# Kernel tuning notes

Hardware: AMD Instinct MI355X
Metric: run time of the kernel (lower is better)

## Reference

```python
import jax, jax.numpy as jnp
import numpy as np

B, L, D, H = 64, 256, 512, 512


def setup_inputs() -> dict:
    key = jax.random.key(0)
    ks = jax.random.split(key, 17)
    s = 1.0 / np.sqrt(D + H)  # torch nn.Linear default init bound

    def w(k):
        return jax.random.uniform(k, (H, D + H), minval=-s, maxval=s, dtype=jnp.float32)

    def b(k):
        return jax.random.uniform(k, (H,), minval=-s, maxval=s, dtype=jnp.float32)

    inp = {"x": jax.random.normal(ks[0], (B, L, D), dtype=jnp.float32)}
    names = ["f", "i", "o", "g"]
    idx = 1
    for d in ("fw", "bw"):
        for n in names:
            kw, kb = jax.random.split(ks[idx])
            inp[f"W_{d}_{n}"] = w(kw)
            inp[f"b_{d}_{n}"] = b(kb)
            idx += 1
    return inp


def _make_cell(Wf, bf, Wi, bi, Wo, bo, Wg, bg):
    def cell(carry, xt):
        h, c = carry
        comb = jnp.concatenate([xt, h], axis=1)  # (B, D+H)
        ft = jax.nn.sigmoid(comb @ Wf.T + bf)
        it = jax.nn.sigmoid(comb @ Wi.T + bi)
        ot = jax.nn.sigmoid(comb @ Wo.T + bo)
        gt = jnp.tanh(comb @ Wg.T + bg)
        c = ft * c + it * gt
        h = ot * jnp.tanh(c)
        return (h, c), h
    return cell


def reference(x, W_fw_f, b_fw_f, W_fw_i, b_fw_i, W_fw_o, b_fw_o, W_fw_g, b_fw_g,
              W_bw_f, b_bw_f, W_bw_i, b_bw_i, W_bw_o, b_bw_o, W_bw_g, b_bw_g):
    Bx, Lx, _ = x.shape
    Hx = W_fw_f.shape[0]
    h0 = jnp.zeros((Bx, Hx), x.dtype)
    c0 = jnp.zeros((Bx, Hx), x.dtype)
    xs = jnp.swapaxes(x, 0, 1)  # (L, B, D) time-major

    _, hf = jax.lax.scan(_make_cell(W_fw_f, b_fw_f, W_fw_i, b_fw_i, W_fw_o, b_fw_o, W_fw_g, b_fw_g), (h0, c0), xs)
    _, hb = jax.lax.scan(_make_cell(W_bw_f, b_bw_f, W_bw_i, b_bw_i, W_bw_o, b_bw_o, W_bw_g, b_bw_g), (h0, c0), xs[::-1])
    hb = hb[::-1]  # hidden_b.reverse() in original

    # Faithful to original: stack time-major, flatten, hstack, reshape(B, L, 2H)
    flat = jnp.concatenate([hf.reshape(-1, Hx), hb.reshape(-1, Hx)], axis=1)  # (L*B, 2H)
    return flat.reshape(Bx, Lx, 2 * Hx)
```

## Files before the change

kernel.cpp:

```cpp
#include <hip/hip_runtime.h>

typedef unsigned short u16;
typedef unsigned int u32;
typedef __bf16 bf16x8 __attribute__((ext_vector_type(8)));
typedef float f32x4 __attribute__((ext_vector_type(4)));

#define OFF_XPROJ 0ull
#define OFF_HBUF  134217728ull
#define OFF_XBF   134479872ull
#define OFF_WXBF  151257088ull
#define OFF_BIAS  155451392ull
#define OFF_FLAGS 155459584ull

struct WPtrs { const float* p[8]; };

__device__ __forceinline__ u16 f2bf(float f) {
    __bf16 h = (__bf16)f;
    return __builtin_bit_cast(u16, h);
}
__device__ __forceinline__ float bf2f(u16 u) {
    __bf16 h = __builtin_bit_cast(__bf16, u);
    return (float)h;
}
__device__ __forceinline__ u32 pack2(float a, float b) {
    return (u32)f2bf(a) | ((u32)f2bf(b) << 16);
}
__device__ __forceinline__ float sigf(float x) {
    return 1.0f / (1.0f + __expf(-x));
}

__global__ void __launch_bounds__(256) pack_x(const float* __restrict__ x, u16* __restrict__ xbf) {
    int idx = blockIdx.x * 256 + threadIdx.x;
    int e = idx * 4;
    float4 v = *(const float4*)(x + e);
    xbf[e+0] = f2bf(v.x); xbf[e+1] = f2bf(v.y);
    xbf[e+2] = f2bf(v.z); xbf[e+3] = f2bf(v.w);
}

__global__ void __launch_bounds__(256) pack_w(WPtrs wp, u16* __restrict__ wxbf) {
    int idx = blockIdx.x * 256 + threadIdx.x;
    int e = idx * 4;
    int n = e >> 9;
    int k = e & 511;
    int j = n & 511, g = (n >> 9) & 3, d = n >> 11;
    const float* W = wp.p[d*4 + g];
    float4 v = *(const float4*)(W + j*1024 + k);
    wxbf[n*512 + k + 0] = f2bf(v.x); wxbf[n*512 + k + 1] = f2bf(v.y);
    wxbf[n*512 + k + 2] = f2bf(v.z); wxbf[n*512 + k + 3] = f2bf(v.w);
}

__global__ void __launch_bounds__(256) pack_bias(WPtrs bp, u16* __restrict__ biasws, unsigned* flagws) {
    int idx = blockIdx.x * 256 + threadIdx.x;
    int j = idx & 511, g = (idx >> 9) & 3, d = idx >> 11;
    biasws[idx] = f2bf(bp.p[d*4 + g][j]);
    if (idx < 1024) flagws[idx] = 0u;
}

__global__ void __launch_bounds__(256) gemm_xproj(const u16* __restrict__ xbf,
                                                  const u16* __restrict__ wxbf,
                                                  const u16* __restrict__ biasws,
                                                  u16* __restrict__ xproj) {
    __shared__ u16 A[64 * 264];
    int tid = threadIdx.x, w = tid >> 6, lane = tid & 63, q = lane >> 4, ln = lane & 15;
    int mb = blockIdx.x >> 6, nb = blockIdx.x & 63;
    int n = nb*64 + w*16 + ln;

    bf16x8 bfr[16];
    #pragma unroll
    for (int kk = 0; kk < 16; ++kk)
        bfr[kk] = *(const bf16x8*)(wxbf + n*512 + kk*32 + q*8);
    float bias = bf2f(biasws[n]);

    f32x4 acc[4] = {{0.f,0.f,0.f,0.f},{0.f,0.f,0.f,0.f},{0.f,0.f,0.f,0.f},{0.f,0.f,0.f,0.f}};
    const u16* Abase = xbf + (size_t)mb * 64 * 512;

    for (int half = 0; half < 2; ++half) {
        for (int it = 0; it < 8; ++it) {
            int idx = tid + it*256;
            int r = idx >> 5, c = idx & 31;
            *(uint4*)&A[r*264 + c*8] = *(const uint4*)(Abase + r*512 + half*256 + c*8);
        }
        __syncthreads();
        #pragma unroll
        for (int kk = 0; kk < 8; ++kk) {
            #pragma unroll
            for (int mt = 0; mt < 4; ++mt) {
                bf16x8 af = *(const bf16x8*)&A[(mt*16 + ln)*264 + kk*32 + q*8];
                acc[mt] = __builtin_amdgcn_mfma_f32_16x16x32_bf16(af, bfr[half*8 + kk], acc[mt], 0, 0, 0);
            }
        }
        __syncthreads();
    }

    int dd = n >> 11, gg = (n >> 9) & 3, jj = n & 511;
    #pragma unroll
    for (int mt = 0; mt < 4; ++mt) {
        #pragma unroll
        for (int r2 = 0; r2 < 4; ++r2) {
            int m = mb*64 + mt*16 + q*4 + r2;
            int t = m & 255, b = m >> 8;
            float v = acc[mt][r2] + bias;
            xproj[(size_t)((dd*256 + t)*64 + b) * 2048 + gg*512 + jj] = f2bf(v);
        }
    }
}

__device__ __forceinline__ void bar_store(unsigned* flags, int cb, int tid, unsigned epoch) {
    if (tid == 0)
        __hip_atomic_store(&flags[cb*16], epoch, __ATOMIC_RELAXED, __HIP_MEMORY_SCOPE_AGENT);
}
__device__ __forceinline__ void bar_wait(unsigned* flags, int tid, unsigned epoch) {
    if (tid < 32) {
        while (__hip_atomic_load(&flags[tid*16], __ATOMIC_RELAXED, __HIP_MEMORY_SCOPE_AGENT) < epoch)
            __builtin_amdgcn_s_sleep(1);
    }
    if (tid == 0)
        (void)__hip_atomic_load(&flags[0], __ATOMIC_ACQUIRE, __HIP_MEMORY_SCOPE_AGENT);
    __syncthreads();
}

__global__ void __launch_bounds__(256) bilstm_rec(const u16* __restrict__ xproj,
                                                  u16* __restrict__ hbuf,
                                                  float* __restrict__ out,
                                                  WPtrs wp, unsigned* flagbase) {
    __shared__ u16 A[64 * 264];
    __shared__ float pre[4 * 64 * 17];
    __shared__ float cst[1024];
    __shared__ u16 xpbuf[4 * 64 * 16];

    int tid = threadIdx.x, w = tid >> 6, lane = tid & 63, q = lane >> 4, ln = lane & 15;
    int d = blockIdx.x >> 5, cb = blockIdx.x & 31, j0 = cb * 16;
    unsigned* flags = flagbase + d*512;
    u32* hb32 = (u32*)hbuf;

    const float* Wg = wp.p[d*4 + w];
    bf16x8 bfr[16];
    #pragma unroll
    for (int kk = 0; kk < 16; ++kk) {
        const float* src = Wg + (j0 + ln)*1024 + 512 + kk*32 + q*8;
        float4 v0 = *(const float4*)src;
        float4 v1 = *(const float4*)(src + 4);
        bf16x8 t;
        t[0]=(__bf16)v0.x; t[1]=(__bf16)v0.y; t[2]=(__bf16)v0.z; t[3]=(__bf16)v0.w;
        t[4]=(__bf16)v1.x; t[5]=(__bf16)v1.y; t[6]=(__bf16)v1.z; t[7]=(__bf16)v1.w;
        bfr[kk] = t;
    }

    #pragma unroll
    for (int k = 0; k < 4; ++k) cst[tid*4 + k] = 0.f;
    #pragma unroll
    for (int i = 0; i < 2; ++i) {
        int dw = tid*2 + i;
        int b = dw >> 3, hcw = dw & 7;
        __hip_atomic_store(&hb32[(d*32768 + b*512 + j0)/2 + hcw], 0u,
                           __ATOMIC_RELAXED, __HIP_MEMORY_SCOPE_AGENT);
    }
    {
        int t0 = d ? 255 : 0;
        const u16* xp_t = xproj + (size_t)((d*256 + t0)*64)*2048 + j0;
        #pragma unroll
        for (int i = 0; i < 2; ++i) {
            int c = tid*2 + i;
            int g = c >> 7, b = (c >> 1) & 63, h8 = c & 1;
            *(uint4*)&xpbuf[c*8] = *(const uint4*)(xp_t + (size_t)b*2048 + g*512 + h8*8);
        }
    }
    __syncthreads();
    bar_store(flags, cb, tid, 1u);
    bar_wait(flags, tid, 1u);

    for (int s = 0; s < 256; ++s) {
        int t_ = d ? (255 - s) : s;
        const u16* hsrc = hbuf + ((s & 1)*2 + d) * 32768;
        f32x4 acc[4] = {{0.f,0.f,0.f,0.f},{0.f,0.f,0.f,0.f},{0.f,0.f,0.f,0.f},{0.f,0.f,0.f,0.f}};

        for (int half = 0; half < 2; ++half) {
            #pragma unroll
            for (int it = 0; it < 8; ++it) {
                int idx = tid + it*256;
                int r = idx >> 5, c = idx & 31;
                *(uint4*)&A[r*264 + c*8] = *(const uint4*)(hsrc + r*512 + half*256 + c*8);
            }
            __syncthreads();
            #pragma unroll
            for (int kk = 0; kk < 8; ++kk) {
                #pragma unroll
                for (int mt = 0; mt < 4; ++mt) {
                    bf16x8 af = *(const bf16x8*)&A[(mt*16 + ln)*264 + kk*32 + q*8];
                    acc[mt] = __builtin_amdgcn_mfma_f32_16x16x32_bf16(af, bfr[half*8 + kk], acc[mt], 0, 0, 0);
                }
            }
            __syncthreads();
        }

        #pragma unroll
        for (int mt = 0; mt < 4; ++mt) {
            #pragma unroll
            for (int r2 = 0; r2 < 4; ++r2)
                pre[w*1088 + (mt*16 + q*4 + r2)*17 + ln] = acc[mt][r2];
        }
        __syncthreads();

        int b = tid >> 2, hc0 = (tid & 3) * 4, p0 = tid * 4;
        int nb_off = (((s + 1) & 1)*2 + d) * 32768;
        float h4[4];
        #pragma unroll
        for (int k = 0; k < 4; ++k) {
            int hc = hc0 + k, p = p0 + k;
            float fpre = pre[0*1088 + b*17 + hc] + bf2f(xpbuf[0*1024 + p]);
            float ipre = pre[1*1088 + b*17 + hc] + bf2f(xpbuf[1*1024 + p]);
            float opre = pre[2*1088 + b*17 + hc] + bf2f(xpbuf[2*1024 + p]);
            float gpre = pre[3*1088 + b*17 + hc] + bf2f(xpbuf[3*1024 + p]);
            float fg = sigf(fpre), ig = sigf(ipre), og = sigf(opre);
            float gg = tanhf(gpre);
            float c = fg * cst[p] + ig * gg;
            cst[p] = c;
            h4[k] = og * tanhf(c);
        }
        int dwbase = (nb_off + b*512 + j0 + hc0) >> 1;
        __hip_atomic_store(&hb32[dwbase],     pack2(h4[0], h4[1]), __ATOMIC_RELAXED, __HIP_MEMORY_SCOPE_AGENT);
        __hip_atomic_store(&hb32[dwbase + 1], pack2(h4[2], h4[3]), __ATOMIC_RELAXED, __HIP_MEMORY_SCOPE_AGENT);

        __syncthreads();
        bar_store(flags, cb, tid, (unsigned)(s + 2));

        f32x4 o4 = { h4[0], h4[1], h4[2], h4[3] };
        __builtin_nontemporal_store(o4, (f32x4*)&out[(size_t)(t_*64 + b)*1024 + d*512 + j0 + hc0]);

        uint4 r0, r1;
        bool havepf = (s + 1 < 256);
        int c0 = tid*2, c1 = tid*2 + 1;
        if (havepf) {
            int tn = d ? (254 - s) : (s + 1);
            const u16* xp_t = xproj + (size_t)((d*256 + tn)*64)*2048 + j0;
            int g0 = c0 >> 7, b0 = (c0 >> 1) & 63, h80 = c0 & 1;
            int g1 = c1 >> 7, b1 = (c1 >> 1) & 63, h81 = c1 & 1;
            r0 = *(const uint4*)(xp_t + (size_t)b0*2048 + g0*512 + h80*8);
            r1 = *(const uint4*)(xp_t + (size_t)b1*2048 + g1*512 + h81*8);
        }

        bar_wait(flags, tid, (unsigned)(s + 2));

        if (havepf) {
            *(uint4*)&xpbuf[c0*8] = r0;
            *(uint4*)&xpbuf[c1*8] = r1;
        }
    }
}

extern "C" void kernel_launch(void* const* d_in, const int* in_sizes, int n_in,
                              void* d_out, int out_size, void* d_ws, size_t ws_size,
                              hipStream_t stream) {
    const float* x = (const float*)d_in[0];
    WPtrs wp, bp;
    for (int d = 0; d < 2; ++d) {
        for (int g = 0; g < 4; ++g) {
            wp.p[d*4 + g] = (const float*)d_in[1 + d*8 + g*2];
            bp.p[d*4 + g] = (const float*)d_in[2 + d*8 + g*2];
        }
    }
    char* ws = (char*)d_ws;
    u16* xproj    = (u16*)(ws + OFF_XPROJ);
    u16* hbuf     = (u16*)(ws + OFF_HBUF);
    u16* xbf      = (u16*)(ws + OFF_XBF);
    u16* wxbf     = (u16*)(ws + OFF_WXBF);
    u16* biasw    = (u16*)(ws + OFF_BIAS);
    unsigned* flg = (unsigned*)(ws + OFF_FLAGS);
    float* out = (float*)d_out;

    hipLaunchKernelGGL(pack_x, dim3(8192), dim3(256), 0, stream, x, xbf);
    hipLaunchKernelGGL(pack_w, dim3(2048), dim3(256), 0, stream, wp, wxbf);
    hipLaunchKernelGGL(pack_bias, dim3(16), dim3(256), 0, stream, bp, biasw, flg);
    hipLaunchKernelGGL(gemm_xproj, dim3(16384), dim3(256), 0, stream,
                       (const u16*)xbf, (const u16*)wxbf, (const u16*)biasw, xproj);

    const u16* xproj_c = xproj;
    void* args[] = { (void*)&xproj_c, (void*)&hbuf, (void*)&out, (void*)&wp, (void*)&flg };
    (void)hipLaunchCooperativeKernel((const void*)bilstm_rec, dim3(64), dim3(256), args, 0, stream);
}
```

Before: 1.686 ms.

## Replace flag barrier with canary-polled hidden-state ring buffer

```diff
diff --git a/kernel.cpp b/kernel.cpp
--- a/kernel.cpp
+++ b/kernel.cpp
@@ -2,15 +2,17 @@
 
 typedef unsigned short u16;
 typedef unsigned int u32;
+typedef unsigned long long u64;
 typedef __bf16 bf16x8 __attribute__((ext_vector_type(8)));
 typedef float f32x4 __attribute__((ext_vector_type(4)));
 
 #define OFF_XPROJ 0ull
-#define OFF_HBUF  134217728ull
-#define OFF_XBF   134479872ull
-#define OFF_WXBF  151257088ull
-#define OFF_BIAS  155451392ull
-#define OFF_FLAGS 155459584ull
+#define OFF_XBF   134217728ull
+#define OFF_WXBF  150994944ull
+#define OFF_BIAS  155189248ull
+#define OFF_HRING 134217728ull
+#define NSLOT 160
+#define RESET_D 8
 
 struct WPtrs { const float* p[8]; };
 
@@ -26,7 +28,16 @@
     return (u32)f2bf(a) | ((u32)f2bf(b) << 16);
 }
 __device__ __forceinline__ float sigf(float x) {
-    return 1.0f / (1.0f + __expf(-x));
+    return __builtin_amdgcn_rcpf(1.0f + __expf(-x));
+}
+__device__ __forceinline__ float tanhfast(float x) {
+    float a = fabsf(x);
+    float e = __expf(-2.0f * a);
+    float t = (1.0f - e) * __builtin_amdgcn_rcpf(1.0f + e);
+    return copysignf(t, x);
+}
+__device__ __forceinline__ bool is_canary(u64 v) {
+    return ((u32)v == 0xFFFFFFFFu) | ((u32)(v >> 32) == 0xFFFFFFFFu);
 }
 
 __global__ void __launch_bounds__(256) pack_x(const float* __restrict__ x, u16* __restrict__ xbf) {
@@ -49,11 +60,20 @@
     wxbf[n*512 + k + 2] = f2bf(v.z); wxbf[n*512 + k + 3] = f2bf(v.w);
 }
 
-__global__ void __launch_bounds__(256) pack_bias(WPtrs bp, u16* __restrict__ biasws, unsigned* flagws) {
+__global__ void __launch_bounds__(256) pack_bias(WPtrs bp, u16* __restrict__ biasws) {
     int idx = blockIdx.x * 256 + threadIdx.x;
     int j = idx & 511, g = (idx >> 9) & 3, d = idx >> 11;
     biasws[idx] = f2bf(bp.p[d*4 + g][j]);
-    if (idx < 1024) flagws[idx] = 0u;
+}
+
+__global__ void __launch_bounds__(256) init_hring(u16* __restrict__ ring) {
+    size_t idx = (size_t)blockIdx.x * 256 + threadIdx.x;
+    size_t byte = idx * 16;
+    size_t seg = byte % 10485760ull;
+    uint4 v;
+    if (seg < 65536ull) { v.x = 0u; v.y = 0u; v.z = 0u; v.w = 0u; }
+    else                { v.x = ~0u; v.y = ~0u; v.z = ~0u; v.w = ~0u; }
+    *(uint4*)((char*)ring + byte) = v;
 }
 
 __global__ void __launch_bounds__(256) gemm_xproj(const u16* __restrict__ xbf,
@@ -105,33 +125,18 @@
     }
 }
 
-__device__ __forceinline__ void bar_store(unsigned* flags, int cb, int tid, unsigned epoch) {
-    if (tid == 0)
-        __hip_atomic_store(&flags[cb*16], epoch, __ATOMIC_RELAXED, __HIP_MEMORY_SCOPE_AGENT);
-}
-__device__ __forceinline__ void bar_wait(unsigned* flags, int tid, unsigned epoch) {
-    if (tid < 32) {
-        while (__hip_atomic_load(&flags[tid*16], __ATOMIC_RELAXED, __HIP_MEMORY_SCOPE_AGENT) < epoch)
-            __builtin_amdgcn_s_sleep(1);
-    }
-    if (tid == 0)
-        (void)__hip_atomic_load(&flags[0], __ATOMIC_ACQUIRE, __HIP_MEMORY_SCOPE_AGENT);
-    __syncthreads();
-}
-
 __global__ void __launch_bounds__(256) bilstm_rec(const u16* __restrict__ xproj,
-                                                  u16* __restrict__ hbuf,
+                                                  u16* __restrict__ hring,
                                                   float* __restrict__ out,
-                                                  WPtrs wp, unsigned* flagbase) {
-    __shared__ u16 A[64 * 264];
+                                                  WPtrs wp) {
+    __shared__ u16 A[64 * 256];
     __shared__ float pre[4 * 64 * 17];
-    __shared__ float cst[1024];
-    __shared__ u16 xpbuf[4 * 64 * 16];
 
     int tid = threadIdx.x, w = tid >> 6, lane = tid & 63, q = lane >> 4, ln = lane & 15;
     int d = blockIdx.x >> 5, cb = blockIdx.x & 31, j0 = cb * 16;
-    unsigned* flags = flagbase + d*512;
-    u32* hb32 = (u32*)hbuf;
+    int b = tid >> 2, hc0 = (tid & 3) * 4;
+    int col8h = tid & 63, rb = tid >> 7;
+    bool phB = (tid & 64) != 0;
 
     const float* Wg = wp.p[d*4 + w];
     bf16x8 bfr[16];
@@ -146,51 +151,91 @@
         bfr[kk] = t;
     }
 
-    #pragma unroll
-    for (int k = 0; k < 4; ++k) cst[tid*4 + k] = 0.f;
-    #pragma unroll
-    for (int i = 0; i < 2; ++i) {
-        int dw = tid*2 + i;
-        int b = dw >> 3, hcw = dw & 7;
-        __hip_atomic_store(&hb32[(d*32768 + b*512 + j0)/2 + hcw], 0u,
-                           __ATOMIC_RELAXED, __HIP_MEMORY_SCOPE_AGENT);
-    }
+    float cre[4] = {0.f, 0.f, 0.f, 0.f};
+
+    u64 xp4[4];
     {
         int t0 = d ? 255 : 0;
-        const u16* xp_t = xproj + (size_t)((d*256 + t0)*64)*2048 + j0;
-        #pragma unroll
-        for (int i = 0; i < 2; ++i) {
-            int c = tid*2 + i;
-            int g = c >> 7, b = (c >> 1) & 63, h8 = c & 1;
-            *(uint4*)&xpbuf[c*8] = *(const uint4*)(xp_t + (size_t)b*2048 + g*512 + h8*8);
-        }
-    }
-    __syncthreads();
-    bar_store(flags, cb, tid, 1u);
-    bar_wait(flags, tid, 1u);
+        const u16* xp_t = xproj + ((size_t)((d*256 + t0)*64 + b))*2048 + j0 + hc0;
+        #pragma unroll
+        for (int g = 0; g < 4; ++g) xp4[g] = *(const u64*)(xp_t + g*512);
+    }
 
     for (int s = 0; s < 256; ++s) {
         int t_ = d ? (255 - s) : s;
-        const u16* hsrc = hbuf + ((s & 1)*2 + d) * 32768;
+        int sl = s;      if (sl >= NSLOT) sl -= NSLOT;
+        int sw = s + 1;  if (sw >= NSLOT) sw -= NSLOT;
+        int sr = s + 1 + RESET_D; if (sr >= NSLOT) sr -= NSLOT;
+        const u64* hsrc = (const u64*)hring + ((size_t)(d*NSLOT + sl)) * 8192;
+
+        u64 vv[32];
+        {
+            u64 v0 = __hip_atomic_load(hsrc + tid, __ATOMIC_RELAXED, __HIP_MEMORY_SCOPE_AGENT);
+            while (is_canary(v0)) {
+                __builtin_amdgcn_s_sleep(1);
+                v0 = __hip_atomic_load(hsrc + tid, __ATOMIC_RELAXED, __HIP_MEMORY_SCOPE_AGENT);
+            }
+            vv[0] = v0;
+        }
+        #pragma unroll
+        for (int it = 1; it < 32; ++it)
+            vv[it] = __hip_atomic_load(hsrc + it*256 + tid, __ATOMIC_RELAXED, __HIP_MEMORY_SCOPE_AGENT);
+        u32 pend = 0;
+        #pragma unroll
+        for (int it = 1; it < 32; ++it)
+            if (is_canary(vv[it])) pend |= (1u << it);
+        while (__builtin_expect(pend != 0u, 0)) {
+            __builtin_amdgcn_s_sleep(1);
+            u32 np = 0;
+            #pragma unroll
+            for (int it = 1; it < 32; ++it)
+                if (pend & (1u << it)) {
+                    u64 v = __hip_atomic_load(hsrc + it*256 + tid, __ATOMIC_RELAXED, __HIP_MEMORY_SCOPE_AGENT);
+                    if (is_canary(v)) np |= (1u << it);
+                    else vv[it] = v;
+                }
+            pend = np;
+        }
+
         f32x4 acc[4] = {{0.f,0.f,0.f,0.f},{0.f,0.f,0.f,0.f},{0.f,0.f,0.f,0.f},{0.f,0.f,0.f,0.f}};
 
-        for (int half = 0; half < 2; ++half) {
-            #pragma unroll
-            for (int it = 0; it < 8; ++it) {
-                int idx = tid + it*256;
-                int r = idx >> 5, c = idx & 31;
-                *(uint4*)&A[r*264 + c*8] = *(const uint4*)(hsrc + r*512 + half*256 + c*8);
-            }
-            __syncthreads();
-            #pragma unroll
-            for (int kk = 0; kk < 8; ++kk) {
-                #pragma unroll
-                for (int mt = 0; mt < 4; ++mt) {
-                    bf16x8 af = *(const bf16x8*)&A[(mt*16 + ln)*264 + kk*32 + q*8];
-                    acc[mt] = __builtin_amdgcn_mfma_f32_16x16x32_bf16(af, bfr[half*8 + kk], acc[mt], 0, 0, 0);
-                }
-            }
-            __syncthreads();
+        if (!phB) {
+            #pragma unroll
+            for (int it = 0; it < 32; ++it) {
+                int row = it*2 + rb;
+                int off = row*512 + ((((col8h >> 1) ^ (row & 7)) << 4) | ((col8h & 1) << 3));
+                *(u64*)((char*)A + off) = vv[it];
+            }
+        }
+        __syncthreads();
+        #pragma unroll
+        for (int kk = 0; kk < 8; ++kk) {
+            #pragma unroll
+            for (int mt = 0; mt < 4; ++mt) {
+                int row = mt*16 + ln;
+                bf16x8 af = *(const bf16x8*)((const char*)A + row*512 + (((kk*4 + q) ^ (ln & 7)) << 4));
+                acc[mt] = __builtin_amdgcn_mfma_f32_16x16x32_bf16(af, bfr[kk], acc[mt], 0, 0, 0);
+            }
+        }
+        __syncthreads();
+
+        if (phB) {
+            #pragma unroll
+            for (int it = 0; it < 32; ++it) {
+                int row = it*2 + rb;
+                int off = row*512 + ((((col8h >> 1) ^ (row & 7)) << 4) | ((col8h & 1) << 3));
+                *(u64*)((char*)A + off) = vv[it];
+            }
+        }
+        __syncthreads();
+        #pragma unroll
+        for (int kk = 0; kk < 8; ++kk) {
+            #pragma unroll
+            for (int mt = 0; mt < 4; ++mt) {
+                int row = mt*16 + ln;
+                bf16x8 af = *(const bf16x8*)((const char*)A + row*512 + (((kk*4 + q) ^ (ln & 7)) << 4));
+                acc[mt] = __builtin_amdgcn_mfma_f32_16x16x32_bf16(af, bfr[8 + kk], acc[mt], 0, 0, 0);
+            }
         }
 
         #pragma unroll
@@ -201,49 +246,38 @@
         }
         __syncthreads();
 
-        int b = tid >> 2, hc0 = (tid & 3) * 4, p0 = tid * 4;
-        int nb_off = (((s + 1) & 1)*2 + d) * 32768;
         float h4[4];
         #pragma unroll
         for (int k = 0; k < 4; ++k) {
-            int hc = hc0 + k, p = p0 + k;
-            float fpre = pre[0*1088 + b*17 + hc] + bf2f(xpbuf[0*1024 + p]);
-            float ipre = pre[1*1088 + b*17 + hc] + bf2f(xpbuf[1*1024 + p]);
-            float opre = pre[2*1088 + b*17 + hc] + bf2f(xpbuf[2*1024 + p]);
-            float gpre = pre[3*1088 + b*17 + hc] + bf2f(xpbuf[3*1024 + p]);
+            int hc = hc0 + k;
+            float fpre = pre[0*1088 + b*17 + hc] + bf2f((u16)(xp4[0] >> (16*k)));
+            float ipre = pre[1*1088 + b*17 + hc] + bf2f((u16)(xp4[1] >> (16*k)));
+            float opre = pre[2*1088 + b*17 + hc] + bf2f((u16)(xp4[2] >> (16*k)));
+            float gpre = pre[3*1088 + b*17 + hc] + bf2f((u16)(xp4[3] >> (16*k)));
             float fg = sigf(fpre), ig = sigf(ipre), og = sigf(opre);
-            float gg = tanhf(gpre);
-            float c = fg * cst[p] + ig * gg;
-            cst[p] = c;
-            h4[k] = og * tanhf(c);
-        }
-        int dwbase = (nb_off + b*512 + j0 + hc0) >> 1;
-        __hip_atomic_store(&hb32[dwbase],     pack2(h4[0], h4[1]), __ATOMIC_RELAXED, __HIP_MEMORY_SCOPE_AGENT);
-        __hip_atomic_store(&hb32[dwbase + 1], pack2(h4[2], h4[3]), __ATOMIC_RELAXED, __HIP_MEMORY_SCOPE_AGENT);
-
-        __syncthreads();
-        bar_store(flags, cb, tid, (unsigned)(s + 2));
+            float gg = tanhfast(gpre);
+            float c = fg * cre[k] + ig * gg;
+            cre[k] = c;
+            h4[k] = og * tanhfast(c);
+        }
+
+        int wi = (b*512 + j0 + hc0) >> 2;
+        {
+            u64* hdst = (u64*)hring + ((size_t)(d*NSLOT + sw)) * 8192;
+            u64 hv = (u64)pack2(h4[0], h4[1]) | ((u64)pack2(h4[2], h4[3]) << 32);
+            __hip_atomic_store(hdst + wi, hv, __ATOMIC_RELAXED, __HIP_MEMORY_SCOPE_AGENT);
+            u64* hrst = (u64*)hring + ((size_t)(d*NSLOT + sr)) * 8192;
+            __hip_atomic_store(hrst + wi, ~0ull, __ATOMIC_RELAXED, __HIP_MEMORY_SCOPE_AGENT);
+        }
 
         f32x4 o4 = { h4[0], h4[1], h4[2], h4[3] };
         __builtin_nontemporal_store(o4, (f32x4*)&out[(size_t)(t_*64 + b)*1024 + d*512 + j0 + hc0]);
 
-        uint4 r0, r1;
-        bool havepf = (s + 1 < 256);
-        int c0 = tid*2, c1 = tid*2 + 1;
-        if (havepf) {
+        if (s + 1 < 256) {
             int tn = d ? (254 - s) : (s + 1);
-            const u16* xp_t = xproj + (size_t)((d*256 + tn)*64)*2048 + j0;
-            int g0 = c0 >> 7, b0 = (c0 >> 1) & 63, h80 = c0 & 1;
-            int g1 = c1 >> 7, b1 = (c1 >> 1) & 63, h81 = c1 & 1;
-            r0 = *(const uint4*)(xp_t + (size_t)b0*2048 + g0*512 + h80*8);
-            r1 = *(const uint4*)(xp_t + (size_t)b1*2048 + g1*512 + h81*8);
-        }
-
-        bar_wait(flags, tid, (unsigned)(s + 2));
-
-        if (havepf) {
-            *(uint4*)&xpbuf[c0*8] = r0;
-            *(uint4*)&xpbuf[c1*8] = r1;
+            const u16* xp_t = xproj + ((size_t)((d*256 + tn)*64 + b))*2048 + j0 + hc0;
+            #pragma unroll
+            for (int g = 0; g < 4; ++g) xp4[g] = *(const u64*)(xp_t + g*512);
         }
     }
 }
@@ -261,20 +295,24 @@
     }
     char* ws = (char*)d_ws;
     u16* xproj    = (u16*)(ws + OFF_XPROJ);
-    u16* hbuf     = (u16*)(ws + OFF_HBUF);
     u16* xbf      = (u16*)(ws + OFF_XBF);
     u16* wxbf     = (u16*)(ws + OFF_WXBF);
     u16* biasw    = (u16*)(ws + OFF_BIAS);
-    unsigned* flg = (unsigned*)(ws + OFF_FLAGS);
+    u16* hring    = (u16*)(ws + OFF_HRING);
     float* out = (float*)d_out;
 
     hipLaunchKernelGGL(pack_x, dim3(8192), dim3(256), 0, stream, x, xbf);
     hipLaunchKernelGGL(pack_w, dim3(2048), dim3(256), 0, stream, wp, wxbf);
-    hipLaunchKernelGGL(pack_bias, dim3(16), dim3(256), 0, stream, bp, biasw, flg);
+    hipLaunchKernelGGL(pack_bias, dim3(16), dim3(256), 0, stream, bp, biasw);
     hipLaunchKernelGGL(gemm_xproj, dim3(16384), dim3(256), 0, stream,
                        (const u16*)xbf, (const u16*)wxbf, (const u16*)biasw, xproj);
+    hipLaunchKernelGGL(init_hring, dim3(5120), dim3(256), 0, stream, hring);
 
     const u16* xproj_c = xproj;
-    void* args[] = { (void*)&xproj_c, (void*)&hbuf, (void*)&out, (void*)&wp, (void*)&flg };
-    (void)hipLaunchCooperativeKernel((const void*)bilstm_rec, dim3(64), dim3(256), args, 0, stream);
-}
+    void* args[] = { (void*)&xproj_c, (void*)&hring, (void*)&out, (void*)&wp };
+    hipError_t err = hipLaunchCooperativeKernel((const void*)bilstm_rec, dim3(64), dim3(256), args, 0, stream);
+    if (err != hipSuccess) {
+        hipLaunchKernelGGL(bilstm_rec, dim3(64), dim3(256), 0, stream,
+                           xproj_c, hring, out, wp);
+    }
+}
```

Result: faster. 1.566 ms (-7.1%).
